# Performance work log

Measured on AMD Instinct MI355X. Metric: run time of the kernel, lower is better.

The kernel has to match this reference:

```python
import jax, jax.numpy as jnp
import numpy as np

N_LAYERS = 2
N_QUBITS = 6
BATCH = 262144
N_CLASSES = 7


def _apply_1q(state, U, w):
    # state: [B, 2]*N_QUBITS (complex); apply 2x2 gate U on wire w (axis w+1)
    s = jnp.moveaxis(state, w + 1, -1)
    s = s @ U.T  # new[a] = sum_b U[a,b] * old[b]
    return jnp.moveaxis(s, -1, w + 1)


def _cnot(state, c, t):
    # flip target axis where control bit == 1
    ax_c, ax_t = c + 1, t + 1
    s0 = jnp.take(state, 0, axis=ax_c)
    s1 = jnp.take(state, 1, axis=ax_c)
    t_ax = ax_t - 1 if ax_t > ax_c else ax_t
    s1 = jnp.flip(s1, axis=t_ax)
    return jnp.stack([s0, s1], axis=ax_c)


def _circuit(x_cont, x_ang, qweights):
    B = x_cont.shape[0]
    # AmplitudeEmbedding(normalize=True) on wires 0,1,2
    amp = x_cont / jnp.linalg.norm(x_cont, axis=1, keepdims=True)  # [B, 8]
    # AngleEmbedding rotation='Y' on wires 3,4,5: RY(th)|0> = cos(th/2)|0> + sin(th/2)|1>
    half = x_ang * 0.5
    q = jnp.stack([jnp.cos(half), jnp.sin(half)], axis=-1)  # [B, 3, 2]
    state = jnp.einsum('bi,bj,bk,bl->bijkl', amp, q[:, 0], q[:, 1], q[:, 2])
    state = state.reshape((B,) + (2,) * N_QUBITS).astype(jnp.complex64)
    # BasicEntanglerLayers: per layer, RX(w) on each wire then CNOT ring
    for l in range(N_LAYERS):
        for w in range(N_QUBITS):
            th = qweights[l, w] * 0.5
            co = jnp.cos(th).astype(jnp.complex64)
            si = (-1j * jnp.sin(th)).astype(jnp.complex64)
            U = jnp.stack([jnp.stack([co, si]), jnp.stack([si, co])])
            state = _apply_1q(state, U, w)
        for w in range(N_QUBITS):
            state = _cnot(state, w, (w + 1) % N_QUBITS)
    # expval PauliZ(0): wire 0 is the leading qubit axis
    sflat = state.reshape(B, 2, 2 ** (N_QUBITS - 1))
    probs = sflat.real ** 2 + sflat.imag ** 2
    return probs[:, 0].sum(axis=1) - probs[:, 1].sum(axis=1)  # [B]


def setup_inputs() -> dict:
    key = jax.random.key(0)
    k1, k2, k3, k4, k5 = jax.random.split(key, 5)
    x_cont = jax.random.normal(k1, (BATCH, 8), jnp.float32)
    x_cat = jax.random.normal(k2, (BATCH, 4), jnp.float32)
    qweights = jax.random.uniform(k3, (N_LAYERS, N_QUBITS), jnp.float32, 0.0, 2.0 * np.pi)
    head_w = jax.random.normal(k4, (N_CLASSES, 1), jnp.float32) * 0.5
    head_b = jax.random.normal(k5, (N_CLASSES,), jnp.float32) * 0.1
    return {'x_cont': x_cont, 'x_cat': x_cat, 'qweights': qweights,
            'head_w': head_w, 'head_b': head_b}


def reference(x_cont, x_cat, qweights, head_w, head_b):
    x_ang = x_cat[:, :3]
    z = _circuit(x_cont, x_ang, qweights)        # [B]
    return z[:, None] @ head_w.T + head_b        # [B, n_classes]
```

## Files before the change

### kernel.cpp

```cpp
#include <hip/hip_runtime.h>
#include <math.h>

#define BATCH 262144
#define NC 7

__global__ __launch_bounds__(256, 4)
void qcirc_kernel(const float* __restrict__ x_cont,
                  const float* __restrict__ x_cat,
                  const float* __restrict__ qw,
                  const float* __restrict__ head_w,
                  const float* __restrict__ head_b,
                  float* __restrict__ out)
{
    const int t = threadIdx.x;
    const int b = blockIdx.x * 256 + t;

    const float4 c0 = *reinterpret_cast<const float4*>(x_cont + b * 8);
    const float4 c1 = *reinterpret_cast<const float4*>(x_cont + b * 8 + 4);
    const float4 xc = *reinterpret_cast<const float4*>(x_cat + b * 4);

    __shared__ float CAB[8];
    __shared__ float HW[8];
    __shared__ float HB[8];
    __shared__ float ZL[256];

    if (t < 7) { HW[t] = head_w[t]; HB[t] = head_b[t]; }

    if (t == 0) {
        float kcv[6], ksv[6];
#pragma unroll
        for (int w = 1; w < 6; ++w) {
            kcv[w] = __cosf(qw[6 + w]);
            ksv[w] = __sinf(qw[6 + w]);
        }
        const float c10 = __cosf(qw[0]), s10 = __sinf(qw[0]);
        const float c11 = __cosf(qw[1]), s11 = __sinf(qw[1]);
        const float c13 = __cosf(qw[3]), s13 = __sinf(qw[3]);
        const float c15 = __cosf(qw[5]), s15 = __sinf(qw[5]);

        const float t3[2] = {c13, -s13};
        const float t5[2] = {c15, -s15};
        const float zc0[2] = {c10, -s10};
        const float zc1[2] = {c11, -s11};
        const float yc0[2] = {s10, c10};
        const float yc1[2] = {s11, c11};
        const float k1[2] = {kcv[1], ksv[1]};
        const float k2[2] = {kcv[2], ksv[2]};
        const float k3[2] = {kcv[3], ksv[3]};
        const float k4[2] = {kcv[4], ksv[4]};
        const float k5[2] = {kcv[5], ksv[5]};

        float W[2][2][2];
#pragma unroll
        for (int m = 0; m < 2; ++m)
#pragma unroll
            for (int y2 = 0; y2 < 2; ++y2)
#pragma unroll
                for (int y5 = 0; y5 < 2; ++y5) {
                    float acc = 0.f;
#pragma unroll
                    for (int y3 = 0; y3 < 2; ++y3) {
                        const int y4 = y3 ^ m;
                        float tt = k3[y3] * k4[y4] * t3[y2 ^ y3] * t5[y4 ^ y5];
                        if ((y2 & y3) ^ (y4 & y5)) tt = -tt;
                        acc += tt;
                    }
                    W[m][y2][y5] = acc;
                }

        float AB[2][2][2] = {};
#pragma unroll
        for (int m = 0; m < 2; ++m)
#pragma unroll
            for (int u2 = 0; u2 < 2; ++u2)
#pragma unroll
                for (int y1 = 0; y1 < 2; ++y1)
#pragma unroll
                    for (int y5 = 0; y5 < 2; ++y5) {
                        const int y2 = y1 ^ u2;
                        float base = k1[y1] * k2[y2] * k5[y5] * W[m][y2][y5];
                        if (y5 && !y1) base = -base;
                        AB[m][0][u2] += base * zc0[y5] * zc1[y1 ^ y5];
                        AB[m][1][u2] += base * yc0[y5] * yc1[y1 ^ y5];
                    }

        CAB[0] = AB[0][0][0];
        CAB[1] = AB[0][0][1] * 2.f;
        CAB[2] = AB[0][1][0] * 2.f;
        CAB[3] = AB[0][1][1] * 2.f;
        CAB[4] = AB[1][0][0];
        CAB[5] = AB[1][0][1] * 2.f;
        CAB[6] = AB[1][1][0] * 2.f;
        CAB[7] = AB[1][1][1] * 2.f;
    }
    __syncthreads();

    const float a0 = c0.x, a1 = c0.y, a2 = c0.z, a3 = c0.w;
    const float a4 = c1.x, a5 = c1.y, a6 = c1.z, a7 = c1.w;

    const float p0 = a0 * a0, p1 = a1 * a1, p2 = a2 * a2, p3 = a3 * a3;
    const float p4 = a4 * a4, p5 = a5 * a5, p6 = a6 * a6, p7 = a7 * a7;
    const float s01 = p0 + p1, s23 = p2 + p3, s45 = p4 + p5, s67 = p6 + p7;
    const float ss = (s01 + s23) + (s45 + s67);

    const float gzz0 = (s01 + s67) - (s23 + s45);
    const float gzz1 = (a0 * a1 + a6 * a7) - (a2 * a3 + a4 * a5);
    const float gyy0 = (a2 * a4 + a3 * a5) - (a0 * a6 + a1 * a7);
    const float gyy1 = (a2 * a5 + a3 * a4) - (a0 * a7 + a1 * a6);

    const float A0 = CAB[0], A1 = CAB[1], A2 = CAB[2], A3 = CAB[3];
    const float B0 = CAB[4], B1 = CAB[5], B2 = CAB[6], B3 = CAB[7];

    const float accA = gzz0 * A0 + gzz1 * A1 + gyy0 * A2 + gyy1 * A3;
    const float accB = gzz0 * B0 + gzz1 * B1 + gyy0 * B2 + gyy1 * B3;

    const float cx0 = __cosf(xc.x);
    const float sx1 = __sinf(xc.y);
    const float cx2 = __cosf(xc.z);

    ZL[t] = cx0 * cx2 * __builtin_amdgcn_rcpf(ss) * fmaf(sx1, accB, accA);
    __syncthreads();

    float* outb = out + (size_t)blockIdx.x * 1792;
#pragma unroll
    for (int rep = 0; rep < 2; ++rep) {
        const int i = rep * 256 + t;
        if (rep == 0 || t < 192) {
            float4 v;
#pragma unroll
            for (int k = 0; k < 4; ++k) {
                const int f = 4 * i + k;
                const int bl = f / 7;
                const int c = f - bl * 7;
                (&v.x)[k] = fmaf(ZL[bl], HW[c], HB[c]);
            }
            *reinterpret_cast<float4*>(outb + 4 * i) = v;
        }
    }
}

extern "C" void kernel_launch(void* const* d_in, const int* in_sizes, int n_in,
                              void* d_out, int out_size, void* d_ws, size_t ws_size,
                              hipStream_t stream) {
    (void)in_sizes; (void)n_in; (void)out_size; (void)d_ws; (void)ws_size;
    const float* x_cont = (const float*)d_in[0];
    const float* x_cat  = (const float*)d_in[1];
    const float* qw     = (const float*)d_in[2];
    const float* head_w = (const float*)d_in[3];
    const float* head_b = (const float*)d_in[4];
    float* out = (float*)d_out;

    const int threads = 256;
    const int blocks = BATCH / threads;
    qcirc_kernel<<<blocks, threads, 0, stream>>>(x_cont, x_cat, qw, head_w, head_b, out);
}
```

Before: 10.05 us.

## Remove block barriers via per-wave coefficient compute and wave-local output staging

Every thread now computes the eight circuit coefficients redundantly instead of thread 0 computing them and sharing them through LDS, which removes the first __syncthreads. Output staging is restricted to each wavefront's own 64 results and its own copy of the head weights, so the second barrier is dropped and the code relies on wave-level lockstep for LDS visibility. Output stores become nontemporal. The trade-off is extra redundant transcendental math per thread, and the code depends on the implicit ordering of LDS accesses within a wavefront.

```diff
diff --git a/kernel.cpp b/kernel.cpp
--- a/kernel.cpp
+++ b/kernel.cpp
@@ -3,6 +3,8 @@
 
 #define BATCH 262144
 #define NC 7
+
+typedef float floatx4 __attribute__((ext_vector_type(4)));
 
 __global__ __launch_bounds__(256, 4)
 void qcirc_kernel(const float* __restrict__ x_cont,
@@ -13,25 +15,26 @@
                   float* __restrict__ out)
 {
     const int t = threadIdx.x;
+    const int w = t >> 6;
+    const int l = t & 63;
     const int b = blockIdx.x * 256 + t;
 
     const float4 c0 = *reinterpret_cast<const float4*>(x_cont + b * 8);
     const float4 c1 = *reinterpret_cast<const float4*>(x_cont + b * 8 + 4);
     const float4 xc = *reinterpret_cast<const float4*>(x_cat + b * 4);
 
-    __shared__ float CAB[8];
-    __shared__ float HW[8];
-    __shared__ float HB[8];
-    __shared__ float ZL[256];
+    __shared__ float  ZL[256];
+    __shared__ float2 HWB[4][8];
 
-    if (t < 7) { HW[t] = head_w[t]; HB[t] = head_b[t]; }
+    if (l < 7) HWB[w][l] = make_float2(head_w[l], head_b[l]);
 
-    if (t == 0) {
+    float CAB[8];
+    {
         float kcv[6], ksv[6];
 #pragma unroll
-        for (int w = 1; w < 6; ++w) {
-            kcv[w] = __cosf(qw[6 + w]);
-            ksv[w] = __sinf(qw[6 + w]);
+        for (int ww = 1; ww < 6; ++ww) {
+            kcv[ww] = __cosf(qw[6 + ww]);
+            ksv[ww] = __sinf(qw[6 + ww]);
         }
         const float c10 = __cosf(qw[0]), s10 = __sinf(qw[0]);
         const float c11 = __cosf(qw[1]), s11 = __sinf(qw[1]);
@@ -93,7 +96,6 @@
         CAB[6] = AB[1][1][0] * 2.f;
         CAB[7] = AB[1][1][1] * 2.f;
     }
-    __syncthreads();
 
     const float a0 = c0.x, a1 = c0.y, a2 = c0.z, a3 = c0.w;
     const float a4 = c1.x, a5 = c1.y, a6 = c1.z, a7 = c1.w;
@@ -108,33 +110,31 @@
     const float gyy0 = (a2 * a4 + a3 * a5) - (a0 * a6 + a1 * a7);
     const float gyy1 = (a2 * a5 + a3 * a4) - (a0 * a7 + a1 * a6);
 
-    const float A0 = CAB[0], A1 = CAB[1], A2 = CAB[2], A3 = CAB[3];
-    const float B0 = CAB[4], B1 = CAB[5], B2 = CAB[6], B3 = CAB[7];
-
-    const float accA = gzz0 * A0 + gzz1 * A1 + gyy0 * A2 + gyy1 * A3;
-    const float accB = gzz0 * B0 + gzz1 * B1 + gyy0 * B2 + gyy1 * B3;
+    const float accA = gzz0 * CAB[0] + gzz1 * CAB[1] + gyy0 * CAB[2] + gyy1 * CAB[3];
+    const float accB = gzz0 * CAB[4] + gzz1 * CAB[5] + gyy0 * CAB[6] + gyy1 * CAB[7];
 
     const float cx0 = __cosf(xc.x);
     const float sx1 = __sinf(xc.y);
     const float cx2 = __cosf(xc.z);
 
     ZL[t] = cx0 * cx2 * __builtin_amdgcn_rcpf(ss) * fmaf(sx1, accB, accA);
-    __syncthreads();
 
-    float* outb = out + (size_t)blockIdx.x * 1792;
+    float* outw = out + (size_t)blockIdx.x * 1792 + w * 448;
 #pragma unroll
     for (int rep = 0; rep < 2; ++rep) {
-        const int i = rep * 256 + t;
-        if (rep == 0 || t < 192) {
-            float4 v;
+        const int j = rep * 64 + l;
+        if (rep == 0 || l < 48) {
+            floatx4 v;
 #pragma unroll
             for (int k = 0; k < 4; ++k) {
-                const int f = 4 * i + k;
-                const int bl = f / 7;
-                const int c = f - bl * 7;
-                (&v.x)[k] = fmaf(ZL[bl], HW[c], HB[c]);
+                const int f = 4 * j + k;
+                const int e = f / 7;
+                const int c = f - e * 7;
+                const float  zz = ZL[(w << 6) + e];
+                const float2 hh = HWB[w][c];
+                v[k] = fmaf(zz, hh.x, hh.y);
             }
-            *reinterpret_cast<float4*>(outb + 4 * i) = v;
+            __builtin_nontemporal_store(v, reinterpret_cast<floatx4*>(outw + 4 * j));
         }
     }
 }
```

Result: no change. 9.999 us (-0.5%).
